# Kernel optimization log

Measured on AMD Instinct MI355X. Metric: run time of the kernel, lower is better.

Reference implementation:

```python
import jax, jax.numpy as jnp
import numpy as np

N = 200000      # active voxels
K = 27          # kernel volume (3x3x3)
M = 50000       # rulebook pairs per kernel offset
CIN = 64
COUT = 64


def setup_inputs() -> dict:
    key = jax.random.key(0)
    k1, k2, k3, k4 = jax.random.split(key, 4)
    feats = jax.random.normal(k1, (N, CIN), dtype=jnp.float32)
    std = 1.0 / np.sqrt(CIN * K)
    kernel = jax.random.uniform(k2, (K, CIN, COUT), dtype=jnp.float32,
                                minval=-std, maxval=std)
    in_map = jax.random.randint(k3, (K, M), 0, N, dtype=jnp.int32)
    out_map = jax.random.randint(k4, (K, M), 0, N, dtype=jnp.int32)
    return {"feats": feats, "kernel": kernel, "in_map": in_map, "out_map": out_map}


def reference(feats, kernel, in_map, out_map):
    # gather: [K, M, Cin]
    gathered = feats[in_map]
    # per-offset GEMM: [K, M, Cout]
    partial = jnp.einsum('kmi,kio->kmo', gathered, kernel)
    # scatter-add into output features [N, Cout]
    out = jnp.zeros((feats.shape[0], kernel.shape[-1]), dtype=feats.dtype)
    out = out.at[out_map].add(partial)
    return out
```

## Files before the change

kernel.cpp:

```cpp
#include <hip/hip_runtime.h>
#include <hip/hip_fp16.h>

#define CIN   64
#define COUT  64

typedef __attribute__((ext_vector_type(8))) short bf16x8;
typedef __attribute__((ext_vector_type(4))) float f32x4;

__device__ inline unsigned short f2bf(float f) {
    unsigned u = __float_as_uint(f);
    return (unsigned short)((u + 0x7FFFu + ((u >> 16) & 1u)) >> 16);
}

__device__ inline unsigned pack_h2(float lo, float hi) {
    __half l = __float2half(lo), h = __float2half(hi);
    return (unsigned)__half_as_ushort(l) | ((unsigned)__half_as_ushort(h) << 16);
}

__device__ inline float2 h2f2(unsigned v) {
    return make_float2(
        __half2float(__ushort_as_half((unsigned short)(v & 0xFFFFu))),
        __half2float(__ushort_as_half((unsigned short)(v >> 16))));
}

__global__ __launch_bounds__(256)
void cvt_hist(const float4* __restrict__ in, unsigned short* __restrict__ outb,
              int n8, const int* __restrict__ out_map, int total,
              int* __restrict__ cnt, int* __restrict__ rk) {
    int i = blockIdx.x * 256 + threadIdx.x;
    if (i < n8) {
        float4 f0 = in[2 * i], f1 = in[2 * i + 1];
        bf16x8 o;
        o[0] = (short)f2bf(f0.x); o[1] = (short)f2bf(f0.y);
        o[2] = (short)f2bf(f0.z); o[3] = (short)f2bf(f0.w);
        o[4] = (short)f2bf(f1.x); o[5] = (short)f2bf(f1.y);
        o[6] = (short)f2bf(f1.z); o[7] = (short)f2bf(f1.w);
        *(bf16x8*)(outb + 8 * (size_t)i) = o;
    }
    if (i < total)
        rk[i] = atomicAdd(&cnt[out_map[i]], 1);
}

__global__ __launch_bounds__(256)
void scanA(const int* __restrict__ cnt, int* __restrict__ excl,
           int* __restrict__ blocksum, int N) {
    __shared__ int sm[256];
    const int b = blockIdx.x, t = threadIdx.x;
    const int base = b * 1024 + t * 4;
    int v0 = (base + 0 < N) ? cnt[base + 0] : 0;
    int v1 = (base + 1 < N) ? cnt[base + 1] : 0;
    int v2 = (base + 2 < N) ? cnt[base + 2] : 0;
    int v3 = (base + 3 < N) ? cnt[base + 3] : 0;
    const int s = v0 + v1 + v2 + v3;
    sm[t] = s; __syncthreads();
    for (int off = 1; off < 256; off <<= 1) {
        int x = (t >= off) ? sm[t - off] : 0;
        __syncthreads();
        sm[t] += x;
        __syncthreads();
    }
    const int e = sm[t] - s;
    if (t == 255) blocksum[b] = sm[t];
    if (base + 0 < N) excl[base + 0] = e;
    if (base + 1 < N) excl[base + 1] = e + v0;
    if (base + 2 < N) excl[base + 2] = e + v0 + v1;
    if (base + 3 < N) excl[base + 3] = e + v0 + v1 + v2;
}

__global__ __launch_bounds__(256)
void scanB(const int* __restrict__ blocksum, int* __restrict__ blockbase,
           int nb, int* __restrict__ total_out) {
    __shared__ int sm[256];
    const int t = threadIdx.x;
    const int s = (t < nb) ? blocksum[t] : 0;
    sm[t] = s; __syncthreads();
    for (int off = 1; off < 256; off <<= 1) {
        int x = (t >= off) ? sm[t - off] : 0;
        __syncthreads();
        sm[t] += x;
        __syncthreads();
    }
    if (t < nb) blockbase[t] = sm[t] - s;
    if (t == 255) *total_out = sm[255];
}

__global__ __launch_bounds__(256)
void scanC(int* __restrict__ offsets, const int* __restrict__ blockbase, int N) {
    int i = blockIdx.x * 256 + threadIdx.x;
    if (i >= N) return;
    offsets[i] += blockbase[i >> 10];
}

__global__ __launch_bounds__(256)
void spconv_phase1(const unsigned short* __restrict__ featsb,
                   const float*          __restrict__ weight,
                   const int*            __restrict__ in_map,
                   const int*            __restrict__ out_map,
                   const int*            __restrict__ offsets,
                   const int*            __restrict__ rk,
                   unsigned*             __restrict__ partial_dw,
                   int M) {
    const int k      = blockIdx.y;
    const int tid    = threadIdx.x;
    const int lane   = tid & 63;
    const int m      = lane & 15;
    const int quad   = lane >> 4;
    const int wave   = blockIdx.x * 4 + (tid >> 6);
    const int nwaves = gridDim.x * 4;

    const float* __restrict__ wk = weight + (size_t)k * (CIN * COUT);
    bf16x8 afrag[4][2];
#pragma unroll
    for (int t = 0; t < 4; ++t) {
        const int n = 16 * (m >> 2) + 4 * t + (m & 3);
#pragma unroll
        for (int h = 0; h < 2; ++h) {
            const int c0 = 32 * h + 8 * quad;
#pragma unroll
            for (int j = 0; j < 8; ++j)
                afrag[t][h][j] = (short)f2bf(wk[(c0 + j) * COUT + n]);
        }
    }

    const int base   = k * M;
    const int ntiles = M >> 4;

    int t0 = wave, t1 = wave + nwaves, t2 = wave + 2 * nwaves;

    int ir0 = 0, orow0 = 0, rk0 = 0;
    if (t0 < ntiles) {
        const int p = base + (t0 << 4) + m;
        ir0 = in_map[p]; orow0 = out_map[p]; rk0 = rk[p];
    }
    int slt0 = 0; bf16x8 a0_0 = {}, a1_0 = {};
    if (t0 < ntiles) {
        if (quad == 0) slt0 = offsets[orow0] + rk0;
        const unsigned short* fb = featsb + ((size_t)ir0 << 6) + 8 * quad;
        a0_0 = *(const bf16x8*)fb;
        a1_0 = *(const bf16x8*)(fb + 32);
    }
    int ir1 = 0, orow1 = 0, rk1 = 0;
    if (t1 < ntiles) {
        const int p = base + (t1 << 4) + m;
        ir1 = in_map[p]; orow1 = out_map[p]; rk1 = rk[p];
    }

    while (t0 < ntiles) {
        int slt1 = 0; bf16x8 a0_1 = {}, a1_1 = {};
        if (t1 < ntiles) {
            if (quad == 0) slt1 = offsets[orow1] + rk1;
            const unsigned short* fb = featsb + ((size_t)ir1 << 6) + 8 * quad;
            a0_1 = *(const bf16x8*)fb;
            a1_1 = *(const bf16x8*)(fb + 32);
        }
        int ir2 = 0, orow2 = 0, rk2 = 0;
        if (t2 < ntiles) {
            const int p = base + (t2 << 4) + m;
            ir2 = in_map[p]; orow2 = out_map[p]; rk2 = rk[p];
        }

        f32x4 acc[4];
#pragma unroll
        for (int t = 0; t < 4; ++t) {
            acc[t] = {0.f, 0.f, 0.f, 0.f};
            acc[t] = __builtin_amdgcn_mfma_f32_16x16x32_bf16(afrag[t][0], a0_0, acc[t], 0, 0, 0);
            acc[t] = __builtin_amdgcn_mfma_f32_16x16x32_bf16(afrag[t][1], a1_0, acc[t], 0, 0, 0);
        }

        const int s = __shfl(slt0, m);
        unsigned d[8];
#pragma unroll
        for (int t = 0; t < 4; ++t) {
            d[2 * t]     = pack_h2(acc[t][0], acc[t][1]);
            d[2 * t + 1] = pack_h2(acc[t][2], acc[t][3]);
        }
        uint4* dst = (uint4*)(partial_dw + (size_t)s * 32 + 8 * quad);
        dst[0] = make_uint4(d[0], d[1], d[2], d[3]);
        dst[1] = make_uint4(d[4], d[5], d[6], d[7]);

        t0 = t1; t1 = t2; t2 += nwaves;
        slt0 = slt1; a0_0 = a0_1; a1_0 = a1_1;
        ir1 = ir2; orow1 = orow2; rk1 = rk2;
    }
}

__global__ __launch_bounds__(256)
void spconv_phase2(const uint4* __restrict__ partial_q,
                   const int*   __restrict__ offsets,
                   float4*      __restrict__ out4,
                   int nrows) {
    const int tid  = threadIdx.x;
    const int lane = tid & 63;
    const int g    = lane >> 3;
    const int q    = lane & 7;
    const int wave = blockIdx.x * 4 + (tid >> 6);
    const int nw   = gridDim.x * 4;

    if (wave >= nrows) return;
    int cur_s = offsets[wave];
    int cur_e = offsets[wave + 1];

    for (int r = wave; r < nrows; r += nw) {
        const int start = cur_s;
        const int c     = cur_e - start;
        const int rn    = r + nw;
        if (rn < nrows) {
            cur_s = offsets[rn];
            cur_e = offsets[rn + 1];
        }

        float s0 = 0.f, s1 = 0.f, s2 = 0.f, s3 = 0.f;
        float s4 = 0.f, s5 = 0.f, s6 = 0.f, s7 = 0.f;
        for (int j0 = 0; j0 < c; j0 += 8) {
            const int j = j0 + g;
            if (j < c) {
                const uint4 v = partial_q[(size_t)(start + j) * 8 + q];
                const float2 f0 = h2f2(v.x), f1 = h2f2(v.y);
                const float2 f2 = h2f2(v.z), f3 = h2f2(v.w);
                s0 += f0.x; s1 += f0.y; s2 += f1.x; s3 += f1.y;
                s4 += f2.x; s5 += f2.y; s6 += f3.x; s7 += f3.y;
            }
        }

#pragma unroll
        for (int msk = 8; msk <= 32; msk <<= 1) {
            s0 += __shfl_xor(s0, msk); s1 += __shfl_xor(s1, msk);
            s2 += __shfl_xor(s2, msk); s3 += __shfl_xor(s3, msk);
            s4 += __shfl_xor(s4, msk); s5 += __shfl_xor(s5, msk);
            s6 += __shfl_xor(s6, msk); s7 += __shfl_xor(s7, msk);
        }

        if (g == 0) {
            out4[(size_t)r * 16 + 2 * q]     = make_float4(s0, s1, s2, s3);
            out4[(size_t)r * 16 + 2 * q + 1] = make_float4(s4, s5, s6, s7);
        }
    }
}

__global__ __launch_bounds__(256)
void spconv_atomic(const float* __restrict__ feats,
                   const float* __restrict__ weight,
                   const int*   __restrict__ in_map,
                   const int*   __restrict__ out_map,
                   float*       __restrict__ out,
                   int M) {
    const int k      = blockIdx.y;
    const int tid    = threadIdx.x;
    const int lane   = tid & 63;
    const int m      = lane & 15;
    const int quad   = lane >> 4;
    const int wave   = blockIdx.x * 4 + (tid >> 6);
    const int nwaves = gridDim.x * 4;

    const float* __restrict__ wk = weight + (size_t)k * (CIN * COUT);
    bf16x8 bfrag[4][2];
#pragma unroll
    for (int t = 0; t < 4; ++t)
#pragma unroll
        for (int h = 0; h < 2; ++h) {
            const int n  = 16 * t + m;
            const int c0 = 32 * h + 8 * quad;
#pragma unroll
            for (int j = 0; j < 8; ++j)
                bfrag[t][h][j] = (short)f2bf(wk[(c0 + j) * COUT + n]);
        }

    const int base   = k * M;
    const int ntiles = M >> 4;

    for (int tile = wave; tile < ntiles; tile += nwaves) {
        const int p0 = tile << 4;
        const int in_row  = in_map[base + p0 + m];
        const int out_row = out_map[base + p0 + m];

        const float* __restrict__ fr = feats + ((size_t)in_row << 6) + 8 * quad;
        const f32x4 f0 = *(const f32x4*)(fr + 0);
        const f32x4 f1 = *(const f32x4*)(fr + 4);
        const f32x4 f2 = *(const f32x4*)(fr + 32);
        const f32x4 f3 = *(const f32x4*)(fr + 36);

        bf16x8 a0, a1;
#pragma unroll
        for (int j = 0; j < 4; ++j) {
            a0[j]     = (short)f2bf(f0[j]);
            a0[j + 4] = (short)f2bf(f1[j]);
            a1[j]     = (short)f2bf(f2[j]);
            a1[j + 4] = (short)f2bf(f3[j]);
        }

        int orow[4];
#pragma unroll
        for (int r = 0; r < 4; ++r)
            orow[r] = __shfl(out_row, 4 * quad + r);

        f32x4 acc[4];
#pragma unroll
        for (int t = 0; t < 4; ++t) {
            acc[t] = {0.f, 0.f, 0.f, 0.f};
            acc[t] = __builtin_amdgcn_mfma_f32_16x16x32_bf16(a0, bfrag[t][0], acc[t], 0, 0, 0);
            acc[t] = __builtin_amdgcn_mfma_f32_16x16x32_bf16(a1, bfrag[t][1], acc[t], 0, 0, 0);
        }

#pragma unroll
        for (int t = 0; t < 4; ++t)
#pragma unroll
            for (int r = 0; r < 4; ++r)
                atomicAdd(out + (size_t)orow[r] * COUT + 16 * t + m, acc[t][r]);
    }
}

__global__ __launch_bounds__(256)
void zero_out_kernel(float4* __restrict__ out, int n4) {
    int i = blockIdx.x * 256 + threadIdx.x;
    if (i < n4) out[i] = make_float4(0.f, 0.f, 0.f, 0.f);
}

static inline size_t al256(size_t x) { return (x + 255) & ~(size_t)255; }

extern "C" void kernel_launch(void* const* d_in, const int* in_sizes, int n_in,
                              void* d_out, int out_size, void* d_ws, size_t ws_size,
                              hipStream_t stream) {
    const float* feats   = (const float*)d_in[0];
    const float* weight  = (const float*)d_in[1];
    const int*   in_map  = (const int*)d_in[2];
    const int*   out_map = (const int*)d_in[3];
    float*       out     = (float*)d_out;

    const int K     = in_sizes[1] / (CIN * COUT);
    const int M     = in_sizes[2] / K;
    const int N     = out_size / COUT;
    const int total = K * M;
    const int nb    = (N + 1023) >> 10;

    const size_t off_b  = al256((size_t)(N + 1) * 4);
    const size_t cnt_b  = al256((size_t)N * 4);
    const size_t bs_b   = al256((size_t)nb * 4);
    const size_t bb_b   = al256((size_t)nb * 4);
    const size_t rank_b = al256((size_t)total * 4);
    const size_t fb_b   = al256((size_t)N * CIN * 2);
    const size_t part_b = (size_t)total * COUT * 2;
    const size_t need   = off_b + cnt_b + bs_b + bb_b + rank_b + fb_b + part_b;

    if ((M & 15) == 0 && nb <= 256 && ws_size >= need) {
        char* p = (char*)d_ws;
        int*            offsets   = (int*)p;            p += off_b;
        int*            cnt       = (int*)p;            p += cnt_b;
        int*            blocksum  = (int*)p;            p += bs_b;
        int*            blockbase = (int*)p;            p += bb_b;
        int*            rk        = (int*)p;            p += rank_b;
        unsigned short* featsb    = (unsigned short*)p; p += fb_b;
        unsigned*       partial   = (unsigned*)p;

        const int n8 = N * CIN / 8;
        const int fused_n = (n8 > total) ? n8 : total;

        hipMemsetAsync(cnt, 0, (size_t)N * 4, stream);
        cvt_hist<<<(fused_n + 255) / 256, 256, 0, stream>>>(
            (const float4*)feats, featsb, n8, out_map, total, cnt, rk);
        scanA<<<nb, 256, 0, stream>>>(cnt, offsets, blocksum, N);
        scanB<<<1, 256, 0, stream>>>(blocksum, blockbase, nb, offsets + N);
        scanC<<<(N + 255) / 256, 256, 0, stream>>>(offsets, blockbase, N);

        dim3 g1(80, K);
        spconv_phase1<<<g1, 256, 0, stream>>>(featsb, weight, in_map, out_map,
                                              offsets, rk, partial, M);

        spconv_phase2<<<8192, 256, 0, stream>>>((const uint4*)partial, offsets,
                                                (float4*)out, N);
        return;
    }

    int n4 = out_size / 4;
    zero_out_kernel<<<(n4 + 255) / 256, 256, 0, stream>>>((float4*)out, n4);
    dim3 grid(80, K);
    spconv_atomic<<<grid, 256, 0, stream>>>(feats, weight, in_map, out_map, out, M);
}
```

Measured before the change: 303.8 us.

## Process two row tiles per wave in phase1 and add nontemporal loads/stores

Phase1 now has each wave handle two 16-row tiles per iteration, an A half and a B half. It loads the rulebook indices for both tiles with all 32 lanes and broadcasts them by shuffle. This doubles the gather loads and MFMA work in flight per wave, which should hide more gather latency. The weight fragment column mapping is permuted so each lane's packed output forms contiguous 16-byte stores, and nontemporal hints are added across the histogram, phase1 and phase2 streams. It raises register pressure, and the tiles are now split into contiguous A and B halves rather than strided, which changes the memory access pattern.

New measurement: 315.8 us. +3.9%, slower.

```diff
diff --git a/kernel.cpp b/kernel.cpp
--- a/kernel.cpp
+++ b/kernel.cpp
@@ -6,6 +6,7 @@
 
 typedef __attribute__((ext_vector_type(8))) short bf16x8;
 typedef __attribute__((ext_vector_type(4))) float f32x4;
+typedef __attribute__((ext_vector_type(4))) unsigned u32x4;
 
 __device__ inline unsigned short f2bf(float f) {
     unsigned u = __float_as_uint(f);
@@ -24,21 +25,25 @@
 }
 
 __global__ __launch_bounds__(256)
-void cvt_hist(const float4* __restrict__ in, unsigned short* __restrict__ outb,
+void cvt_hist(const f32x4* __restrict__ in, unsigned short* __restrict__ outb,
               int n8, const int* __restrict__ out_map, int total,
               int* __restrict__ cnt, int* __restrict__ rk) {
     int i = blockIdx.x * 256 + threadIdx.x;
     if (i < n8) {
-        float4 f0 = in[2 * i], f1 = in[2 * i + 1];
+        f32x4 f0 = __builtin_nontemporal_load(&in[2 * i]);
+        f32x4 f1 = __builtin_nontemporal_load(&in[2 * i + 1]);
         bf16x8 o;
-        o[0] = (short)f2bf(f0.x); o[1] = (short)f2bf(f0.y);
-        o[2] = (short)f2bf(f0.z); o[3] = (short)f2bf(f0.w);
-        o[4] = (short)f2bf(f1.x); o[5] = (short)f2bf(f1.y);
-        o[6] = (short)f2bf(f1.z); o[7] = (short)f2bf(f1.w);
+        o[0] = (short)f2bf(f0[0]); o[1] = (short)f2bf(f0[1]);
+        o[2] = (short)f2bf(f0[2]); o[3] = (short)f2bf(f0[3]);
+        o[4] = (short)f2bf(f1[0]); o[5] = (short)f2bf(f1[1]);
+        o[6] = (short)f2bf(f1[2]); o[7] = (short)f2bf(f1[3]);
         *(bf16x8*)(outb + 8 * (size_t)i) = o;
     }
-    if (i < total)
-        rk[i] = atomicAdd(&cnt[out_map[i]], 1);
+    if (i < total) {
+        const int om = __builtin_nontemporal_load(&out_map[i]);
+        const int r  = atomicAdd(&cnt[om], 1);
+        __builtin_nontemporal_store(r, &rk[i]);
+    }
 }
 
 __global__ __launch_bounds__(256)
@@ -112,7 +117,7 @@
     bf16x8 afrag[4][2];
 #pragma unroll
     for (int t = 0; t < 4; ++t) {
-        const int n = 16 * (m >> 2) + 4 * t + (m & 3);
+        const int n = 32 * (t >> 1) + 8 * (m >> 2) + 4 * (t & 1) + (m & 3);
 #pragma unroll
         for (int h = 0; h < 2; ++h) {
             const int c0 = 32 * h + 8 * quad;
@@ -124,68 +129,114 @@
 
     const int base   = k * M;
     const int ntiles = M >> 4;
-
-    int t0 = wave, t1 = wave + nwaves, t2 = wave + 2 * nwaves;
-
-    int ir0 = 0, orow0 = 0, rk0 = 0;
-    if (t0 < ntiles) {
-        const int p = base + (t0 << 4) + m;
-        ir0 = in_map[p]; orow0 = out_map[p]; rk0 = rk[p];
-    }
-    int slt0 = 0; bf16x8 a0_0 = {}, a1_0 = {};
-    if (t0 < ntiles) {
-        if (quad == 0) slt0 = offsets[orow0] + rk0;
-        const unsigned short* fb = featsb + ((size_t)ir0 << 6) + 8 * quad;
-        a0_0 = *(const bf16x8*)fb;
-        a1_0 = *(const bf16x8*)(fb + 32);
-    }
-    int ir1 = 0, orow1 = 0, rk1 = 0;
-    if (t1 < ntiles) {
-        const int p = base + (t1 << 4) + m;
-        ir1 = in_map[p]; orow1 = out_map[p]; rk1 = rk[p];
-    }
-
-    while (t0 < ntiles) {
-        int slt1 = 0; bf16x8 a0_1 = {}, a1_1 = {};
-        if (t1 < ntiles) {
-            if (quad == 0) slt1 = offsets[orow1] + rk1;
-            const unsigned short* fb = featsb + ((size_t)ir1 << 6) + 8 * quad;
-            a0_1 = *(const bf16x8*)fb;
-            a1_1 = *(const bf16x8*)(fb + 32);
-        }
-        int ir2 = 0, orow2 = 0, rk2 = 0;
-        if (t2 < ntiles) {
-            const int p = base + (t2 << 4) + m;
-            ir2 = in_map[p]; orow2 = out_map[p]; rk2 = rk[p];
-        }
-
-        f32x4 acc[4];
-#pragma unroll
-        for (int t = 0; t < 4; ++t) {
-            acc[t] = {0.f, 0.f, 0.f, 0.f};
-            acc[t] = __builtin_amdgcn_mfma_f32_16x16x32_bf16(afrag[t][0], a0_0, acc[t], 0, 0, 0);
-            acc[t] = __builtin_amdgcn_mfma_f32_16x16x32_bf16(afrag[t][1], a1_0, acc[t], 0, 0, 0);
-        }
-
-        const int s = __shfl(slt0, m);
-        unsigned d[8];
-#pragma unroll
-        for (int t = 0; t < 4; ++t) {
-            d[2 * t]     = pack_h2(acc[t][0], acc[t][1]);
-            d[2 * t + 1] = pack_h2(acc[t][2], acc[t][3]);
-        }
-        uint4* dst = (uint4*)(partial_dw + (size_t)s * 32 + 8 * quad);
-        dst[0] = make_uint4(d[0], d[1], d[2], d[3]);
-        dst[1] = make_uint4(d[4], d[5], d[6], d[7]);
-
-        t0 = t1; t1 = t2; t2 += nwaves;
-        slt0 = slt1; a0_0 = a0_1; a1_0 = a1_1;
-        ir1 = ir2; orow1 = orow2; rk1 = rk2;
-    }
-}
-
-__global__ __launch_bounds__(256)
-void spconv_phase2(const uint4* __restrict__ partial_q,
+    const int nA     = (ntiles + 1) >> 1;
+    const int nB     = ntiles - nA;
+
+    const int lh  = lane & 31;
+    const int sel = lh >> 4;
+    const int em  = lh & 15;
+
+    auto load_maps = [&](int p, int& ir, int& orow, int& rkv) {
+        const bool v = sel ? (p < nB) : (p < nA);
+        const int  t = sel ? (nA + p) : p;
+        const int  a = v ? (base + (t << 4) + em) : base;
+        ir   = __builtin_nontemporal_load(in_map  + a);
+        orow = __builtin_nontemporal_load(out_map + a);
+        rkv  = __builtin_nontemporal_load(rk      + a);
+    };
+
+    int p0 = wave, p1 = wave + nwaves, p2 = wave + 2 * nwaves;
+
+    int    ir1 = 0, or1 = 0, rv1 = 0;
+    int    slt0 = 0;
+    bf16x8 aA0_0 = {}, aA1_0 = {}, aB0_0 = {}, aB1_0 = {};
+
+    if (p0 < nA) {
+        int ir0, or0, rv0;
+        load_maps(p0, ir0, or0, rv0);
+        slt0 = offsets[or0] + rv0;
+        const int irA = __shfl(ir0, m);
+        const int irB = __shfl(ir0, m + 16);
+        const unsigned short* fa = featsb + ((size_t)irA << 6) + 8 * quad;
+        aA0_0 = *(const bf16x8*)fa;
+        aA1_0 = *(const bf16x8*)(fa + 32);
+        const unsigned short* fb = featsb + ((size_t)irB << 6) + 8 * quad;
+        aB0_0 = *(const bf16x8*)fb;
+        aB1_0 = *(const bf16x8*)(fb + 32);
+        if (p1 < nA) load_maps(p1, ir1, or1, rv1);
+    }
+
+    while (p0 < nA) {
+        int    slt1 = 0;
+        bf16x8 aA0_1 = {}, aA1_1 = {}, aB0_1 = {}, aB1_1 = {};
+        if (p1 < nA) {
+            slt1 = offsets[or1] + rv1;
+            const int irA = __shfl(ir1, m);
+            const int irB = __shfl(ir1, m + 16);
+            const unsigned short* fa = featsb + ((size_t)irA << 6) + 8 * quad;
+            aA0_1 = *(const bf16x8*)fa;
+            aA1_1 = *(const bf16x8*)(fa + 32);
+            const unsigned short* fb = featsb + ((size_t)irB << 6) + 8 * quad;
+            aB0_1 = *(const bf16x8*)fb;
+            aB1_1 = *(const bf16x8*)(fb + 32);
+        }
+        int ir2 = 0, or2 = 0, rv2 = 0;
+        if (p2 < nA) load_maps(p2, ir2, or2, rv2);
+
+        {
+            f32x4 acc[4];
+#pragma unroll
+            for (int t = 0; t < 4; ++t) {
+                acc[t] = {0.f, 0.f, 0.f, 0.f};
+                acc[t] = __builtin_amdgcn_mfma_f32_16x16x32_bf16(afrag[t][0], aA0_0, acc[t], 0, 0, 0);
+                acc[t] = __builtin_amdgcn_mfma_f32_16x16x32_bf16(afrag[t][1], aA1_0, acc[t], 0, 0, 0);
+            }
+            const int s = __shfl(slt0, m);
+            u32x4 w0, w1;
+            w0[0] = pack_h2(acc[0][0], acc[0][1]);
+            w0[1] = pack_h2(acc[0][2], acc[0][3]);
+            w0[2] = pack_h2(acc[1][0], acc[1][1]);
+            w0[3] = pack_h2(acc[1][2], acc[1][3]);
+            w1[0] = pack_h2(acc[2][0], acc[2][1]);
+            w1[1] = pack_h2(acc[2][2], acc[2][3]);
+            w1[2] = pack_h2(acc[3][0], acc[3][1]);
+            w1[3] = pack_h2(acc[3][2], acc[3][3]);
+            unsigned* bp = partial_dw + (size_t)s * 32 + 4 * quad;
+            __builtin_nontemporal_store(w0, (u32x4*)bp);
+            __builtin_nontemporal_store(w1, (u32x4*)(bp + 16));
+        }
+        if (p0 < nB) {
+            f32x4 acc[4];
+#pragma unroll
+            for (int t = 0; t < 4; ++t) {
+                acc[t] = {0.f, 0.f, 0.f, 0.f};
+                acc[t] = __builtin_amdgcn_mfma_f32_16x16x32_bf16(afrag[t][0], aB0_0, acc[t], 0, 0, 0);
+                acc[t] = __builtin_amdgcn_mfma_f32_16x16x32_bf16(afrag[t][1], aB1_0, acc[t], 0, 0, 0);
+            }
+            const int s = __shfl(slt0, m + 16);
+            u32x4 w0, w1;
+            w0[0] = pack_h2(acc[0][0], acc[0][1]);
+            w0[1] = pack_h2(acc[0][2], acc[0][3]);
+            w0[2] = pack_h2(acc[1][0], acc[1][1]);
+            w0[3] = pack_h2(acc[1][2], acc[1][3]);
+            w1[0] = pack_h2(acc[2][0], acc[2][1]);
+            w1[1] = pack_h2(acc[2][2], acc[2][3]);
+            w1[2] = pack_h2(acc[3][0], acc[3][1]);
+            w1[3] = pack_h2(acc[3][2], acc[3][3]);
+            unsigned* bp = partial_dw + (size_t)s * 32 + 4 * quad;
+            __builtin_nontemporal_store(w0, (u32x4*)bp);
+            __builtin_nontemporal_store(w1, (u32x4*)(bp + 16));
+        }
+
+        p0 = p1; p1 = p2; p2 += nwaves;
+        slt0 = slt1;
+        aA0_0 = aA0_1; aA1_0 = aA1_1; aB0_0 = aB0_1; aB1_0 = aB1_1;
+        ir1 = ir2; or1 = or2; rv1 = rv2;
+    }
+}
+
+__global__ __launch_bounds__(256)
+void spconv_phase2(const u32x4* __restrict__ partial_q,
                    const int*   __restrict__ offsets,
                    float4*      __restrict__ out4,
                    int nrows) {
@@ -214,9 +265,10 @@
         for (int j0 = 0; j0 < c; j0 += 8) {
             const int j = j0 + g;
             if (j < c) {
-                const uint4 v = partial_q[(size_t)(start + j) * 8 + q];
-                const float2 f0 = h2f2(v.x), f1 = h2f2(v.y);
-                const float2 f2 = h2f2(v.z), f3 = h2f2(v.w);
+                const u32x4 v = __builtin_nontemporal_load(
+                    &partial_q[(size_t)(start + j) * 8 + q]);
+                const float2 f0 = h2f2(v[0]), f1 = h2f2(v[1]);
+                const float2 f2 = h2f2(v[2]), f3 = h2f2(v[3]);
                 s0 += f0.x; s1 += f0.y; s2 += f1.x; s3 += f1.y;
                 s4 += f2.x; s5 += f2.y; s6 += f3.x; s7 += f3.y;
             }
@@ -354,9 +406,9 @@
         const int n8 = N * CIN / 8;
         const int fused_n = (n8 > total) ? n8 : total;
 
-        hipMemsetAsync(cnt, 0, (size_t)N * 4, stream);
+        (void)hipMemsetAsync(cnt, 0, (size_t)N * 4, stream);
         cvt_hist<<<(fused_n + 255) / 256, 256, 0, stream>>>(
-            (const float4*)feats, featsb, n8, out_map, total, cnt, rk);
+            (const f32x4*)feats, featsb, n8, out_map, total, cnt, rk);
         scanA<<<nb, 256, 0, stream>>>(cnt, offsets, blocksum, N);
         scanB<<<1, 256, 0, stream>>>(blocksum, blockbase, nb, offsets + N);
         scanC<<<(N + 255) / 256, 256, 0, stream>>>(offsets, blockbase, N);
@@ -365,7 +417,7 @@
         spconv_phase1<<<g1, 256, 0, stream>>>(featsb, weight, in_map, out_map,
                                               offsets, rk, partial, M);
 
-        spconv_phase2<<<8192, 256, 0, stream>>>((const uint4*)partial, offsets,
+        spconv_phase2<<<8192, 256, 0, stream>>>((const u32x4*)partial, offsets,
                                                 (float4*)out, N);
         return;
     }
```
